# Kernel optimization log

Measured on AMD Instinct MI355X. Metric: run time of the kernel, lower is better.

The kernel has to match this reference:

```python
import jax, jax.numpy as jnp
import numpy as np

N = 100000   # nodes
E = 1000000  # edges
IN = 100     # input feature dim
H = 4        # heads
D = 32       # hidden per head (H*D = 128)
C = 47       # classes
EPS = 1e-5
SLOPE = 0.2  # DGL GATv2 leaky_relu negative slope


def setup_inputs() -> dict:
    key = jax.random.key(0)
    ks = jax.random.split(key, 32)
    lin = lambda k, i, o: (jax.random.normal(k, (i, o), jnp.float32) / np.float32(np.sqrt(i)))
    inp = {}
    inp['x'] = jax.random.normal(ks[0], (N, IN), jnp.float32)
    inp['src'] = jax.random.randint(ks[1], (E,), 0, N, jnp.int32)
    inp['dst'] = jnp.sort(jax.random.randint(ks[2], (E,), 0, N, jnp.int32))
    # layer 0: IN -> H*D, Linear residual (IN != H*D)
    inp['Wsrc0'] = lin(ks[3], IN, H * D); inp['bsrc0'] = jnp.zeros(H * D, jnp.float32)
    inp['Wdst0'] = lin(ks[4], IN, H * D); inp['bdst0'] = jnp.zeros(H * D, jnp.float32)
    inp['attn0'] = lin(ks[5], H, D)
    inp['Wres0'] = lin(ks[6], IN, H * D); inp['bres0'] = jnp.zeros(H * D, jnp.float32)
    # layer 1: H*D -> H*D, Identity residual (128 == 128)
    inp['Wsrc1'] = lin(ks[7], H * D, H * D); inp['bsrc1'] = jnp.zeros(H * D, jnp.float32)
    inp['Wdst1'] = lin(ks[8], H * D, H * D); inp['bdst1'] = jnp.zeros(H * D, jnp.float32)
    inp['attn1'] = lin(ks[9], H, D)
    # layer 2: H*D -> H*C, Linear residual (128 != 188)
    inp['Wsrc2'] = lin(ks[10], H * D, H * C); inp['bsrc2'] = jnp.zeros(H * C, jnp.float32)
    inp['Wdst2'] = lin(ks[11], H * D, H * C); inp['bdst2'] = jnp.zeros(H * C, jnp.float32)
    inp['attn2'] = lin(ks[12], H, C)
    inp['Wres2'] = lin(ks[13], H * D, H * C); inp['bres2'] = jnp.zeros(H * C, jnp.float32)
    # BatchNorm1d params (training-mode batch stats)
    inp['g0'] = jnp.ones(H * D, jnp.float32); inp['be0'] = jnp.zeros(H * D, jnp.float32)
    inp['g1'] = jnp.ones(H * D, jnp.float32); inp['be1'] = jnp.zeros(H * D, jnp.float32)
    return inp


def _gatv2(h, src, dst, Ws, bs, Wd, bd, attn, resval):
    """One GATv2Conv on a full block (src feats == dst feats == h)."""
    Hh, Dd = attn.shape
    fs = (h @ Ws + bs).reshape(-1, Hh, Dd)   # [N,H,D] src projection
    fd = (h @ Wd + bd).reshape(-1, Hh, Dd)   # [N,H,D] dst projection
    e = jax.nn.leaky_relu(fs[src] + fd[dst], SLOPE)         # [E,H,D]
    logits = jnp.einsum('ehd,hd->eh', e, attn)              # [E,H]
    m = jax.ops.segment_max(logits, dst, num_segments=N)    # per-dst max
    ex = jnp.exp(logits - m[dst])
    s = jax.ops.segment_sum(ex, dst, num_segments=N)
    alpha = ex / s[dst]                                      # edge softmax
    out = jax.ops.segment_sum(alpha[:, :, None] * fs[src], dst, num_segments=N)
    return out + resval                                      # [N,H,D]


def _bn(x, g, b):
    mu = x.mean(0)
    v = x.var(0)  # biased, as torch BN training mode
    return g * (x - mu) / jnp.sqrt(v + EPS) + b


def reference(x, src, dst,
              Wsrc0, bsrc0, Wdst0, bdst0, attn0, Wres0, bres0,
              Wsrc1, bsrc1, Wdst1, bdst1, attn1,
              Wsrc2, bsrc2, Wdst2, bdst2, attn2, Wres2, bres2,
              g0, be0, g1, be1):
    # layer 0: conv(+relu activation) -> flatten -> BN -> relu (dropout = eval identity)
    res0 = (x @ Wres0 + bres0).reshape(N, H, D)
    h = jax.nn.relu(_gatv2(x, src, dst, Wsrc0, bsrc0, Wdst0, bdst0, attn0, res0))
    h = jax.nn.relu(_bn(h.reshape(N, H * D), g0, be0))
    # layer 1: Identity residual
    res1 = h.reshape(N, H, D)
    h = jax.nn.relu(_gatv2(h, src, dst, Wsrc1, bsrc1, Wdst1, bdst1, attn1, res1))
    h = jax.nn.relu(_bn(h.reshape(N, H * D), g1, be1))
    # layer 2: no activation; mean over heads; log_softmax
    res2 = (h @ Wres2 + bres2).reshape(N, H, C)
    h = _gatv2(h, src, dst, Wsrc2, bsrc2, Wdst2, bdst2, attn2, res2)
    h = h.mean(1)                                # [N,C]
    return jax.nn.log_softmax(h, axis=-1)
```

## Files before the change

kernel.cpp:

```cpp
#include <hip/hip_runtime.h>
#include <hip/hip_bf16.h>

#define Nn 100000
#define Ee 1000000
#define INF_ 100
#define Hh 4
#define Dd 32
#define HD 128
#define Cc 47
#define HC 188
#define HCP 192
#define EPSV 1e-5f
#define SLOPE 0.2f
#define NBLK ((Nn + 255) / 256)

typedef __hip_bfloat16 bf16;
typedef __attribute__((ext_vector_type(8))) short short8;
typedef __attribute__((ext_vector_type(4))) float f32x4;
typedef __attribute__((ext_vector_type(2))) float f32x2;

__device__ __forceinline__ float tof(bf16 v) { return __bfloat162float(v); }
__device__ __forceinline__ float b2f(unsigned short u) {
    return __uint_as_float((unsigned)u << 16);
}
__device__ __forceinline__ float b2flo(unsigned u) {
    return __uint_as_float(u << 16);
}
__device__ __forceinline__ float b2fhi(unsigned u) {
    return __uint_as_float(u & 0xFFFF0000u);
}
__device__ __forceinline__ float ldb(const bf16* p) {
    return b2f(*(const unsigned short*)p);
}
__device__ __forceinline__ unsigned short f2u(float v) {
    bf16 t = __float2bfloat16(v);
    return *(unsigned short*)&t;
}
__device__ __forceinline__ f32x2 pk2(float x, float y) {
    f32x2 r; r.x = x; r.y = y; return r;
}
__device__ __forceinline__ f32x2 pabs2(f32x2 v) {
    return __builtin_elementwise_max(v, -v);
}
__device__ __forceinline__ f32x2 pfma2(f32x2 a, f32x2 b, f32x2 c) {
    return __builtin_elementwise_fma(a, b, c);
}

template <int C>
__device__ __forceinline__ float dppadd(float v) {
    int m = __builtin_amdgcn_update_dpp(0, __float_as_int(v), C, 0xF, 0xF, false);
    return v + __int_as_float(m);
}
template <int C>
__device__ __forceinline__ float dppmax(float v) {
    int m = __builtin_amdgcn_update_dpp(0, __float_as_int(v), C, 0xF, 0xF, false);
    return fmaxf(v, __int_as_float(m));
}
__device__ __forceinline__ float sum16(float p) {
    p = dppadd<0xB1>(p);
    p = dppadd<0x4E>(p);
    p = dppadd<0x124>(p);
    p = dppadd<0x128>(p);
    return p;
}
__device__ __forceinline__ float max16(float p) {
    p = dppmax<0xB1>(p); p = dppmax<0x4E>(p);
    p = dppmax<0x124>(p); p = dppmax<0x128>(p);
    return p;
}

#define L2E 1.4426950408889634f

__global__ void detect_dtype(const unsigned* __restrict__ x, int* __restrict__ flag) {
    if (blockIdx.x == 0 && threadIdx.x == 0) {
        int good = 0;
        for (int i = 0; i < 256; ++i) {
            unsigned lo = x[i] & 0xFFFFu;
            float v = __uint_as_float(lo << 16);
            float a = fabsf(v);
            if (a > 1e-4f && a < 10.f) good++;
        }
        *flag = (good >= 128) ? 1 : 0;
    }
}

__device__ __forceinline__ float ld_any(const void* p, int i, int isbf) {
    return isbf ? tof(((const bf16*)p)[i]) : ((const float*)p)[i];
}

__global__ void cvt_x(const void* __restrict__ in, bf16* __restrict__ out,
                      const int* __restrict__ flag) {
    int i = blockIdx.x * blockDim.x + threadIdx.x;
    if (i >= Nn * 128) return;
    int row = i >> 7, col = i & 127;
    float v = (col < INF_) ? ld_any(in, row * INF_ + col, *flag) : 0.f;
    out[i] = __float2bfloat16(v);
}

#define NSP 15
struct CvtTab { const void* src[NSP]; int off[NSP + 1]; };

__global__ void cvt_params(CvtTab t, bf16* __restrict__ out, int total,
                           const int* __restrict__ flag) {
    int i = blockIdx.x * blockDim.x + threadIdx.x;
    if (i >= total) return;
    int isbf = *flag;
    int seg = 0;
    while (i >= t.off[seg + 1]) seg++;
    out[i] = __float2bfloat16(ld_any(t.src[seg], i - t.off[seg], isbf));
}

#define WROWS 1280
struct PrepTab { const void* src[8]; int row0[8]; int K[8]; int M[8]; int MP[8]; };

__global__ void prep_all(PrepTab t, bf16* __restrict__ wtb, const int* __restrict__ flag) {
    int i = blockIdx.x * blockDim.x + threadIdx.x;
    if (i >= WROWS * 128) return;
    int row = i >> 7, k = i & 127;
    int isbf = *flag;
    float v = 0.f;
#pragma unroll
    for (int q = 0; q < 8; ++q) {
        if (row >= t.row0[q] && row < t.row0[q] + t.MP[q]) {
            int m = row - t.row0[q];
            if (m < t.M[q] && k < t.K[q])
                v = ld_any(t.src[q], k * t.M[q] + m, isbf);
        }
    }
    wtb[i] = __float2bfloat16(v);
}

__global__ void zero_u32(unsigned* __restrict__ p, int n) {
    int i = blockIdx.x * blockDim.x + threadIdx.x;
    if (i < n) p[i] = 0u;
}

__global__ void src_scale_ptr(const int* __restrict__ src, const int* __restrict__ dst,
                              unsigned* __restrict__ w384, unsigned* __restrict__ w256,
                              int* __restrict__ ptr) {
    int i = blockIdx.x * blockDim.x + threadIdx.x;
    if (i < Ee) {
        unsigned s = (unsigned)src[i];
        w384[i] = s * 384u;
        w256[i] = s << 8;
    }
    if (i <= Nn) {
        if (i == Nn) { ptr[Nn] = Ee; return; }
        int lo = 0, hi = Ee;
        while (lo < hi) {
            int mid = (lo + hi) >> 1;
            if (dst[mid] < i) lo = mid + 1; else hi = mid;
        }
        ptr[i] = lo;
    }
}

__global__ void deg_hist_blk(const int* __restrict__ ptr, int* __restrict__ cnt) {
    __shared__ int lh[256];
    int t = threadIdx.x;
    lh[t] = 0;
    __syncthreads();
    int n = blockIdx.x * 256 + t;
    if (n < Nn) {
        int dg = ptr[n + 1] - ptr[n]; if (dg > 255) dg = 255;
        atomicAdd(&lh[dg], 1);
    }
    __syncthreads();
    cnt[t * NBLK + blockIdx.x] = lh[t];
}

__global__ void deg_totals(const int* __restrict__ cnt, int* __restrict__ totals) {
    int wave = threadIdx.x >> 6, lane = threadIdx.x & 63;
    int bin = blockIdx.x * 4 + wave;
    int s = 0;
    for (int k = lane; k < NBLK; k += 64) s += cnt[bin * NBLK + k];
#pragma unroll
    for (int o = 1; o < 64; o <<= 1) s += __shfl_xor(s, o);
    if (lane == 0) totals[bin] = s;
}

__global__ void deg_bases(const int* __restrict__ cnt, const int* __restrict__ totals,
                          int* __restrict__ base) {
    int wave = threadIdx.x >> 6, lane = threadIdx.x & 63;
    int bin = blockIdx.x * 4 + wave;
    int bb = 0;
    for (int b = bin + 1 + lane; b < 256; b += 64) bb += totals[b];
#pragma unroll
    for (int o = 1; o < 64; o <<= 1) bb += __shfl_xor(bb, o);
    int run = bb;
    for (int k0 = 0; k0 < NBLK; k0 += 64) {
        int k = k0 + lane;
        int c = (k < NBLK) ? cnt[bin * NBLK + k] : 0;
        int p = c;
#pragma unroll
        for (int o = 1; o < 64; o <<= 1) {
            int t = __shfl_up(p, o);
            if (lane >= o) p += t;
        }
        if (k < NBLK) base[bin * NBLK + k] = run + (p - c);
        run += __shfl(p, 63);
    }
}

__global__ void deg_scatter_blk(const int* __restrict__ ptr, const int* __restrict__ base,
                                int* __restrict__ perm) {
    __shared__ int lh[256];
    int t = threadIdx.x;
    lh[t] = 0;
    __syncthreads();
    int n = blockIdx.x * 256 + t;
    if (n < Nn) {
        int dg = ptr[n + 1] - ptr[n]; if (dg > 255) dg = 255;
        int loc = atomicAdd(&lh[dg], 1);
        perm[base[dg * NBLK + blockIdx.x] + loc] = n;
    }
}

template <int MP, int NOUT, int CS, bool ABN, bool PACK, int OSTR>
__global__ __launch_bounds__(256, 4) void gemm_big(
    const bf16* __restrict__ A, const bf16* __restrict__ Wt,
    const bf16* __restrict__ b0, const bf16* __restrict__ b1,
    const bf16* __restrict__ b2,
    bf16* __restrict__ o0, bf16* __restrict__ o1, bf16* __restrict__ o2,
    int MR, const float* __restrict__ bnp) {
    __shared__ __align__(16) bf16 Al[64 * 136];
    const int row0 = blockIdx.x * 64;
    const int tid = threadIdx.x;
#pragma unroll
    for (int j = 0; j < 4; ++j) {
        int idx = tid + j * 256;
        int r = idx >> 4, kk = (idx & 15) * 8;
        int4 val = {0, 0, 0, 0};
        if (row0 + r < Nn) {
            val = *(const int4*)&A[(size_t)(row0 + r) * 128 + kk];
            if (ABN) {
                short8 av = *(short8*)&val;
                bf16 tmp[8];
#pragma unroll
                for (int u = 0; u < 8; ++u) {
                    float v = b2f((unsigned short)av[u]);
                    v = fmaxf(fmaf(v, bnp[kk + u], bnp[128 + kk + u]), 0.f);
                    tmp[u] = __float2bfloat16(v);
                }
                val = *(int4*)tmp;
            }
        }
        *(int4*)&Al[r * 136 + kk] = val;
    }
    __syncthreads();
    const int wave = tid >> 6, lane = tid & 63;
    const int n16 = lane & 15, quad = lane >> 4;
    const int colbase = blockIdx.y * (64 * CS) + wave * (16 * CS);
    f32x4 acc[4][CS];
#pragma unroll
    for (int rt = 0; rt < 4; ++rt)
#pragma unroll
        for (int c = 0; c < CS; ++c) acc[rt][c] = (f32x4){0.f, 0.f, 0.f, 0.f};
    const bf16* wb[CS];
#pragma unroll
    for (int c = 0; c < CS; ++c)
        wb[c] = Wt + (size_t)(colbase + c * 16 + n16) * 128 + quad * 8;
    const bf16* ap = Al + n16 * 136 + quad * 8;
#pragma unroll
    for (int ks = 0; ks < 4; ++ks) {
        short8 bf[CS];
#pragma unroll
        for (int c = 0; c < CS; ++c) bf[c] = *(const short8*)(wb[c] + ks * 32);
#pragma unroll
        for (int rt = 0; rt < 4; ++rt) {
            short8 af = *(const short8*)(ap + rt * 16 * 136 + ks * 32);
#pragma unroll
            for (int c = 0; c < CS; ++c)
                acc[rt][c] = __builtin_amdgcn_mfma_f32_16x16x32_bf16(af, bf[c], acc[rt][c], 0, 0, 0);
        }
    }
#pragma unroll
    for (int c = 0; c < CS; ++c) {
        int col = colbase + c * 16 + n16;
        int oi = col / MP, lc = col - oi * MP;
        if (oi >= NOUT || lc >= MR) continue;
        const bf16* bp = (oi == 0) ? b0 : (oi == 1) ? b1 : b2;
        bf16* o = (oi == 0) ? o0 : (oi == 1) ? o1 : o2;
        float bb = tof(bp[lc]);
        int st;
        if (PACK) {
            int hh = lc / 47, cc = lc - hh * 47;
            int jj = cc & 15, kk2 = cc >> 4;
            int l = hh * 16 + jj;
            st = (kk2 < 2) ? (2 * l + kk2) : (128 + l);
        } else {
            st = lc;
        }
#pragma unroll
        for (int rt = 0; rt < 4; ++rt) {
#pragma unroll
            for (int i = 0; i < 4; ++i) {
                int row = row0 + rt * 16 + quad * 4 + i;
                if (row < Nn)
                    o[(size_t)row * OSTR + st] = __float2bfloat16(acc[rt][c][i] + bb);
            }
        }
    }
}

template <bool RESBN>
__global__ __launch_bounds__(256) void gat_fused_128(
    const bf16* __restrict__ fs, const bf16* __restrict__ fd,
    const unsigned* __restrict__ srcW, const int* __restrict__ ptr,
    const int* __restrict__ perm,
    const bf16* __restrict__ attn, const bf16* __restrict__ resb,
    const float* __restrict__ bnp, bf16* __restrict__ hout) {
    const int wave = threadIdx.x >> 6, lane = threadIdx.x & 63;
    const int di = blockIdx.x * 4 + wave;
    if (di >= Nn) return;
    const int d = perm[di];
    const int c0 = lane * 2;
    const unsigned c0b = (unsigned)c0 * 2u;
    ushort2 aq = *(const ushort2*)&attn[c0];
    float a0 = b2f(aq.x) * L2E, a1 = b2f(aq.y) * L2E;
    const f32x2 Av = pk2(0.6f * a0, 0.6f * a1);
    const f32x2 Bv = pk2(0.4f * a0, 0.4f * a1);
    ushort2 dq = *(const ushort2*)&fd[(size_t)d * HD + c0];
    const f32x2 fdv = pk2(b2f(dq.x), b2f(dq.y));
    const char* fsb = (const char*)fs;
    float l = 0.f;
    f32x2 Ov = pk2(0.f, 0.f);
    int e = ptr[d];
    const int e1 = ptr[d + 1];
    for (; e + 3 < e1; e += 4) {
        unsigned vA = srcW[e] + c0b, vB = srcW[e + 1] + c0b;
        unsigned vC = srcW[e + 2] + c0b, vD = srcW[e + 3] + c0b;
        ushort2 qA = *(const ushort2*)(fsb + vA);
        ushort2 qB = *(const ushort2*)(fsb + vB);
        ushort2 qC = *(const ushort2*)(fsb + vC);
        ushort2 qD = *(const ushort2*)(fsb + vD);
        f32x2 fA = pk2(b2f(qA.x), b2f(qA.y));
        f32x2 fB = pk2(b2f(qB.x), b2f(qB.y));
        f32x2 fC = pk2(b2f(qC.x), b2f(qC.y));
        f32x2 fD = pk2(b2f(qD.x), b2f(qD.y));
        f32x2 xA = fA + fdv, xB = fB + fdv, xC = fC + fdv, xD = fD + fdv;
        f32x2 tA = pfma2(pabs2(xA), Bv, xA * Av);
        f32x2 tB = pfma2(pabs2(xB), Bv, xB * Av);
        f32x2 tC = pfma2(pabs2(xC), Bv, xC * Av);
        f32x2 tD = pfma2(pabs2(xD), Bv, xD * Av);
        float pA = tA.x + tA.y, pB = tB.x + tB.y;
        float pC = tC.x + tC.y, pD = tD.x + tD.y;
        pA = sum16(pA); pB = sum16(pB); pC = sum16(pC); pD = sum16(pD);
        float eA = __builtin_amdgcn_exp2f(pA), eB = __builtin_amdgcn_exp2f(pB);
        float eC = __builtin_amdgcn_exp2f(pC), eD = __builtin_amdgcn_exp2f(pD);
        l += (eA + eB) + (eC + eD);
        Ov = pfma2(pk2(eA, eA), fA, Ov);
        Ov = pfma2(pk2(eB, eB), fB, Ov);
        Ov = pfma2(pk2(eC, eC), fC, Ov);
        Ov = pfma2(pk2(eD, eD), fD, Ov);
    }
    for (; e < e1; ++e) {
        unsigned v = srcW[e] + c0b;
        ushort2 fq = *(const ushort2*)(fsb + v);
        f32x2 f = pk2(b2f(fq.x), b2f(fq.y));
        f32x2 x = f + fdv;
        f32x2 t = pfma2(pabs2(x), Bv, x * Av);
        float p = sum16(t.x + t.y);
        float pe = __builtin_amdgcn_exp2f(p);
        l += pe;
        Ov = pfma2(pk2(pe, pe), f, Ov);
    }
    float inv = l > 0.f ? 1.f / l : 0.f;
    ushort2 rq = *(const ushort2*)&resb[(size_t)d * HD + c0];
    float r0 = b2f(rq.x), r1 = b2f(rq.y);
    if (RESBN) {
        r0 = fmaxf(fmaf(r0, bnp[c0], bnp[HD + c0]), 0.f);
        r1 = fmaxf(fmaf(r1, bnp[c0 + 1], bnp[HD + c0 + 1]), 0.f);
    }
    float v0 = fmaxf(fmaf(Ov.x, inv, r0), 0.f);
    float v1 = fmaxf(fmaf(Ov.y, inv, r1), 0.f);
    ushort2 ov; ov.x = f2u(v0); ov.y = f2u(v1);
    *(ushort2*)&hout[(size_t)d * HD + c0] = ov;
}

__global__ __launch_bounds__(256) void gat_fused_188(
    const bf16* __restrict__ fs, const bf16* __restrict__ fd,
    const unsigned* __restrict__ srcW, const int* __restrict__ ptr,
    const int* __restrict__ perm,
    const bf16* __restrict__ attn, const bf16* __restrict__ rs,
    void* __restrict__ out, const int* __restrict__ flag) {
    const int wave = threadIdx.x >> 6, lane = threadIdx.x & 63;
    const int di = blockIdx.x * 4 + wave;
    if (di >= Nn) return;
    const int d = perm[di];
    const int h = lane >> 4, j = lane & 15;
    const unsigned cbA = (unsigned)lane * 4u;
    const unsigned cbB = 256u + (unsigned)lane * 2u;
    const int ca = h * Cc + j;
    const bool has2 = (j < 15);
    float a0 = ldb(&attn[ca]) * L2E;
    float a1 = ldb(&attn[ca + 16]) * L2E;
    float a2 = has2 ? ldb(&attn[ca + 32]) * L2E : 0.f;
    const f32x2 Av = pk2(0.6f * a0, 0.6f * a1);
    const f32x2 Bv = pk2(0.4f * a0, 0.4f * a1);
    const float A2 = 0.6f * a2, B2 = 0.4f * a2;
    const char* fdb = (const char*)fd;
    const size_t drow = (size_t)d * 384u;
    unsigned dqa = *(const unsigned*)(fdb + drow + cbA);
    unsigned short dqb = *(const unsigned short*)(fdb + drow + cbB);
    const f32x2 fdv = pk2(b2flo(dqa), b2fhi(dqa));
    const float fd2 = b2f(dqb);
    const char* fsb = (const char*)fs;
    float l = 0.f, O2 = 0.f;
    f32x2 Ov = pk2(0.f, 0.f);
    int e = ptr[d];
    const int e1 = ptr[d + 1];
    for (; e + 3 < e1; e += 4) {
        unsigned bA = srcW[e], bB = srcW[e + 1], bC = srcW[e + 2], bD = srcW[e + 3];
        unsigned qA = *(const unsigned*)(fsb + bA + cbA);
        unsigned qB = *(const unsigned*)(fsb + bB + cbA);
        unsigned qC = *(const unsigned*)(fsb + bC + cbA);
        unsigned qD = *(const unsigned*)(fsb + bD + cbA);
        unsigned short uA = *(const unsigned short*)(fsb + bA + cbB);
        unsigned short uB = *(const unsigned short*)(fsb + bB + cbB);
        unsigned short uC = *(const unsigned short*)(fsb + bC + cbB);
        unsigned short uD = *(const unsigned short*)(fsb + bD + cbB);
        f32x2 fA = pk2(b2flo(qA), b2fhi(qA)); float gA = b2f(uA);
        f32x2 fB = pk2(b2flo(qB), b2fhi(qB)); float gB = b2f(uB);
        f32x2 fC = pk2(b2flo(qC), b2fhi(qC)); float gC = b2f(uC);
        f32x2 fD = pk2(b2flo(qD), b2fhi(qD)); float gD = b2f(uD);
        f32x2 xA = fA + fdv, xB = fB + fdv, xC = fC + fdv, xD = fD + fdv;
        float yA = gA + fd2, yB = gB + fd2, yC = gC + fd2, yD = gD + fd2;
        f32x2 tA = pfma2(pabs2(xA), Bv, xA * Av);
        f32x2 tB = pfma2(pabs2(xB), Bv, xB * Av);
        f32x2 tC = pfma2(pabs2(xC), Bv, xC * Av);
        f32x2 tD = pfma2(pabs2(xD), Bv, xD * Av);
        float pA = fmaf(yA, A2, fmaf(fabsf(yA), B2, tA.x + tA.y));
        float pB = fmaf(yB, A2, fmaf(fabsf(yB), B2, tB.x + tB.y));
        float pC = fmaf(yC, A2, fmaf(fabsf(yC), B2, tC.x + tC.y));
        float pD = fmaf(yD, A2, fmaf(fabsf(yD), B2, tD.x + tD.y));
        pA = sum16(pA); pB = sum16(pB); pC = sum16(pC); pD = sum16(pD);
        float eA = __builtin_amdgcn_exp2f(pA), eB = __builtin_amdgcn_exp2f(pB);
        float eC = __builtin_amdgcn_exp2f(pC), eD = __builtin_amdgcn_exp2f(pD);
        l += (eA + eB) + (eC + eD);
        Ov = pfma2(pk2(eA, eA), fA, Ov); O2 = fmaf(eA, gA, O2);
        Ov = pfma2(pk2(eB, eB), fB, Ov); O2 = fmaf(eB, gB, O2);
        Ov = pfma2(pk2(eC, eC), fC, Ov); O2 = fmaf(eC, gC, O2);
        Ov = pfma2(pk2(eD, eD), fD, Ov); O2 = fmaf(eD, gD, O2);
    }
    for (; e < e1; ++e) {
        unsigned b = srcW[e];
        unsigned q = *(const unsigned*)(fsb + b + cbA);
        unsigned short u = *(const unsigned short*)(fsb + b + cbB);
        f32x2 f = pk2(b2flo(q), b2fhi(q)); float g = b2f(u);
        f32x2 x = f + fdv;
        float y = g + fd2;
        f32x2 t = pfma2(pabs2(x), Bv, x * Av);
        float p = fmaf(y, A2, fmaf(fabsf(y), B2, t.x + t.y));
        p = sum16(p);
        float pe = __builtin_amdgcn_exp2f(p);
        l += pe;
        Ov = pfma2(pk2(pe, pe), f, Ov); O2 = fmaf(pe, g, O2);
    }
    float inv = l > 0.f ? 1.f / l : 0.f;
    const char* rb_ = (const char*)rs;
    unsigned rqa = *(const unsigned*)(rb_ + drow + cbA);
    unsigned short rqb = *(const unsigned short*)(rb_ + drow + cbB);
    float v0 = fmaf(Ov.x, inv, b2flo(rqa));
    float v1 = fmaf(Ov.y, inv, b2fhi(rqa));
    float v2 = has2 ? fmaf(O2, inv, b2f(rqb)) : 0.f;
    v0 += __shfl_xor(v0, 16); v0 += __shfl_xor(v0, 32); v0 *= 0.25f;
    v1 += __shfl_xor(v1, 16); v1 += __shfl_xor(v1, 32); v1 *= 0.25f;
    v2 += __shfl_xor(v2, 16); v2 += __shfl_xor(v2, 32); v2 *= 0.25f;
    float mx = fmaxf(v0, v1);
    if (has2) mx = fmaxf(mx, v2);
    mx = max16(mx);
    float sm = __expf(v0 - mx) + __expf(v1 - mx) + (has2 ? __expf(v2 - mx) : 0.f);
    sm = sum16(sm);
    if (h == 0) {
        float ls = mx + logf(sm);
        if (*flag) {
            bf16* o = (bf16*)out + (size_t)d * Cc;
            o[j] = __float2bfloat16(v0 - ls);
            o[j + 16] = __float2bfloat16(v1 - ls);
            if (has2) o[j + 32] = __float2bfloat16(v2 - ls);
        } else {
            float* o = (float*)out + (size_t)d * Cc;
            o[j] = v0 - ls;
            o[j + 16] = v1 - ls;
            if (has2) o[j + 32] = v2 - ls;
        }
    }
}

__global__ void col_stats(const bf16* __restrict__ in, float* __restrict__ sums) {
    int c = threadIdx.x;
    int r0 = blockIdx.x * 256;
    int r1 = r0 + 256; if (r1 > Nn) r1 = Nn;
    float s = 0.f, s2 = 0.f;
    for (int r = r0; r < r1; ++r) {
        float v = ldb(&in[(size_t)r * HD + c]);
        s += v; s2 += v * v;
    }
    atomicAdd(&sums[c], s);
    atomicAdd(&sums[HD + c], s2);
}

__global__ void bn_finalize(const float* __restrict__ sums, const bf16* __restrict__ g,
                            const bf16* __restrict__ be, float* __restrict__ ss) {
    int c = threadIdx.x;
    float mu = sums[c] * (1.f / Nn);
    float var = sums[HD + c] * (1.f / Nn) - mu * mu;
    float sc = tof(g[c]) * rsqrtf(var + EPSV);
    ss[c] = sc;
    ss[HD + c] = tof(be[c]) - mu * sc;
}

extern "C" void kernel_launch(void* const* d_in, const int* in_sizes, int n_in,
                              void* d_out, int out_size, void* d_ws, size_t ws_size,
                              hipStream_t stream) {
    (void)in_sizes; (void)n_in; (void)out_size; (void)ws_size;
    const void* x = d_in[0];
    const int* src = (const int*)d_in[1];
    const int* dst = (const int*)d_in[2];

    char* ws = (char*)d_ws;
    size_t off = 0;
    auto alloc = [&](size_t bytes) {
        void* p = ws + off;
        off += (bytes + 255) & ~(size_t)255;
        return p;
    };
    bf16* xb = (bf16*)alloc((size_t)Nn * 128 * 2);
    bf16* rb = (bf16*)alloc((size_t)Nn * HD * 2);
    bf16* rs = xb;
    bf16* fs = (bf16*)alloc((size_t)Nn * HCP * 2);
    bf16* fd = (bf16*)alloc((size_t)Nn * HCP * 2);
    bf16* hbA = (bf16*)alloc((size_t)Nn * HD * 2);
    bf16* hbB = (bf16*)alloc((size_t)Nn * HD * 2);
    int* ptr = (int*)alloc((Nn + 1) * 4);
    bf16* wtb = (bf16*)alloc((size_t)WROWS * 128 * 2);
    float* bns = (float*)alloc(2 * HD * 4);
    float* bnss0 = (float*)alloc(2 * HD * 4);
    float* bnss1 = (float*)alloc(2 * HD * 4);
    bf16* pb = (bf16*)alloc(4096 * 2);
    int* flag = (int*)alloc(256);
    unsigned* w384 = (unsigned*)alloc((size_t)Ee * 4);
    unsigned* w256 = (unsigned*)alloc((size_t)Ee * 4);
    int* cnt = (int*)alloc((size_t)256 * NBLK * 4);
    int* cbase = (int*)alloc((size_t)256 * NBLK * 4);
    int* totals = (int*)alloc(256 * 4);
    int* perm = (int*)alloc((size_t)Nn * 4);

    static const int spIdx[NSP] = {4, 6, 7, 9, 11, 13, 14, 16, 18, 19, 21, 22, 23, 24, 25};
    static const int spSz[NSP]  = {HD, HD, HD, HD, HD, HD, HD, HC, HC, HC, HC, HD, HD, HD, HD};
    CvtTab tab;
    int tot = 0;
    for (int i = 0; i < NSP; ++i) { tab.src[i] = d_in[spIdx[i]]; tab.off[i] = tot; tot += spSz[i]; }
    tab.off[NSP] = tot;
    const bf16 *bsrc0 = pb + tab.off[0], *bdst0 = pb + tab.off[1], *attn0 = pb + tab.off[2],
               *bres0 = pb + tab.off[3], *bsrc1 = pb + tab.off[4], *bdst1 = pb + tab.off[5],
               *attn1 = pb + tab.off[6], *bsrc2 = pb + tab.off[7], *bdst2 = pb + tab.off[8],
               *attn2 = pb + tab.off[9], *bres2 = pb + tab.off[10],
               *g0 = pb + tab.off[11], *be0 = pb + tab.off[12],
               *g1 = pb + tab.off[13], *be1 = pb + tab.off[14];

    PrepTab pt;
    static const int wIdx[8] = {3, 5, 8, 10, 12, 15, 17, 20};
    static const int wK[8]   = {INF_, INF_, INF_, HD, HD, HD, HD, HD};
    static const int wM[8]   = {HD, HD, HD, HD, HD, HC, HC, HC};
    static const int wMP[8]  = {128, 128, 128, 128, 128, 192, 192, 192};
    static const int wR0[8]  = {0, 128, 256, 384, 512, 640, 832, 1024};
    for (int i = 0; i < 8; ++i) {
        pt.src[i] = d_in[wIdx[i]]; pt.row0[i] = wR0[i];
        pt.K[i] = wK[i]; pt.M[i] = wM[i]; pt.MP[i] = wMP[i];
    }

    detect_dtype<<<1, 64, 0, stream>>>((const unsigned*)x, flag);
    cvt_x<<<(Nn * 128 + 255) / 256, 256, 0, stream>>>(x, xb, flag);
    cvt_params<<<(tot + 255) / 256, 256, 0, stream>>>(tab, pb, tot, flag);
    prep_all<<<(WROWS * 128 + 255) / 256, 256, 0, stream>>>(pt, wtb, flag);
    src_scale_ptr<<<(Ee + 255) / 256, 256, 0, stream>>>(src, dst, w384, w256, ptr);
    deg_hist_blk<<<NBLK, 256, 0, stream>>>(ptr, cnt);
    deg_totals<<<64, 256, 0, stream>>>(cnt, totals);
    deg_bases<<<64, 256, 0, stream>>>(cnt, totals, cbase);
    deg_scatter_blk<<<NBLK, 256, 0, stream>>>(ptr, cbase, perm);

    const int fusedGrid = (Nn + 3) / 4;
    const int statsGrid = NBLK;
    const int rowBlk = (Nn + 63) / 64;

    gemm_big<128, 3, 3, false, false, HD><<<dim3(rowBlk, 2), 256, 0, stream>>>(
        xb, wtb, bsrc0, bdst0, bres0, fs, fd, rb, HD, nullptr);
    gat_fused_128<false><<<fusedGrid, 256, 0, stream>>>(fs, fd, w256, ptr, perm,
                                                        attn0, rb, nullptr, hbA);
    zero_u32<<<1, 256, 0, stream>>>((unsigned*)bns, 2 * HD);
    col_stats<<<statsGrid, 128, 0, stream>>>(hbA, bns);
    bn_finalize<<<1, HD, 0, stream>>>(bns, g0, be0, bnss0);

    gemm_big<128, 2, 2, true, false, HD><<<dim3(rowBlk, 2), 256, 0, stream>>>(
        hbA, wtb + (size_t)384 * 128, bsrc1, bdst1, nullptr, fs, fd, nullptr, HD, bnss0);
    gat_fused_128<true><<<fusedGrid, 256, 0, stream>>>(fs, fd, w256, ptr, perm,
                                                       attn1, hbA, bnss0, hbB);
    zero_u32<<<1, 256, 0, stream>>>((unsigned*)bns, 2 * HD);
    col_stats<<<statsGrid, 128, 0, stream>>>(hbB, bns);
    bn_finalize<<<1, HD, 0, stream>>>(bns, g1, be1, bnss1);

    gemm_big<192, 3, 3, true, true, HCP><<<dim3(rowBlk, 3), 256, 0, stream>>>(
        hbB, wtb + (size_t)640 * 128, bsrc2, bdst2, bres2, fs, fd, rs, HC, bnss1);
    gat_fused_188<<<fusedGrid, 256, 0, stream>>>(fs, fd, w384, ptr, perm, attn2, rs,
                                                 d_out, flag);
}
```

Before: 663.9 us.

## Loop column tiles inside GEMM blocks, vectorize edge index loads, use fast log

The GEMM kernel now loops over all column tiles inside one block rather than spreading them across grid.y. The A tile is loaded, and BN-transformed, into LDS once per row block instead of once per column tile, at the cost of a smaller grid and more serial work per block. The GAT aggregation kernels peel edges until the index is 4-aligned so the four source indices can be read with one uint4 load. The final log_softmax uses __log2f times ln2 in place of logf.

```diff
diff --git a/kernel.cpp b/kernel.cpp
--- a/kernel.cpp
+++ b/kernel.cpp
@@ -70,6 +70,7 @@
 }
 
 #define L2E 1.4426950408889634f
+#define LN2 0.6931471805599453f
 
 __global__ void detect_dtype(const unsigned* __restrict__ x, int* __restrict__ flag) {
     if (blockIdx.x == 0 && threadIdx.x == 0) {
@@ -216,7 +217,7 @@
     }
 }
 
-template <int MP, int NOUT, int CS, bool ABN, bool PACK, int OSTR>
+template <int MP, int NOUT, int CS, bool ABN, bool PACK, int OSTR, int NY>
 __global__ __launch_bounds__(256, 4) void gemm_big(
     const bf16* __restrict__ A, const bf16* __restrict__ Wt,
     const bf16* __restrict__ b0, const bf16* __restrict__ b1,
@@ -250,54 +251,57 @@
     __syncthreads();
     const int wave = tid >> 6, lane = tid & 63;
     const int n16 = lane & 15, quad = lane >> 4;
-    const int colbase = blockIdx.y * (64 * CS) + wave * (16 * CS);
-    f32x4 acc[4][CS];
-#pragma unroll
-    for (int rt = 0; rt < 4; ++rt)
-#pragma unroll
-        for (int c = 0; c < CS; ++c) acc[rt][c] = (f32x4){0.f, 0.f, 0.f, 0.f};
-    const bf16* wb[CS];
-#pragma unroll
-    for (int c = 0; c < CS; ++c)
-        wb[c] = Wt + (size_t)(colbase + c * 16 + n16) * 128 + quad * 8;
     const bf16* ap = Al + n16 * 136 + quad * 8;
 #pragma unroll
-    for (int ks = 0; ks < 4; ++ks) {
-        short8 bf[CS];
-#pragma unroll
-        for (int c = 0; c < CS; ++c) bf[c] = *(const short8*)(wb[c] + ks * 32);
-#pragma unroll
-        for (int rt = 0; rt < 4; ++rt) {
-            short8 af = *(const short8*)(ap + rt * 16 * 136 + ks * 32);
-#pragma unroll
-            for (int c = 0; c < CS; ++c)
-                acc[rt][c] = __builtin_amdgcn_mfma_f32_16x16x32_bf16(af, bf[c], acc[rt][c], 0, 0, 0);
-        }
-    }
-#pragma unroll
-    for (int c = 0; c < CS; ++c) {
-        int col = colbase + c * 16 + n16;
-        int oi = col / MP, lc = col - oi * MP;
-        if (oi >= NOUT || lc >= MR) continue;
-        const bf16* bp = (oi == 0) ? b0 : (oi == 1) ? b1 : b2;
-        bf16* o = (oi == 0) ? o0 : (oi == 1) ? o1 : o2;
-        float bb = tof(bp[lc]);
-        int st;
-        if (PACK) {
-            int hh = lc / 47, cc = lc - hh * 47;
-            int jj = cc & 15, kk2 = cc >> 4;
-            int l = hh * 16 + jj;
-            st = (kk2 < 2) ? (2 * l + kk2) : (128 + l);
-        } else {
-            st = lc;
-        }
-#pragma unroll
-        for (int rt = 0; rt < 4; ++rt) {
-#pragma unroll
-            for (int i = 0; i < 4; ++i) {
-                int row = row0 + rt * 16 + quad * 4 + i;
-                if (row < Nn)
-                    o[(size_t)row * OSTR + st] = __float2bfloat16(acc[rt][c][i] + bb);
+    for (int ny = 0; ny < NY; ++ny) {
+        const int colbase = ny * (64 * CS) + wave * (16 * CS);
+        f32x4 acc[4][CS];
+#pragma unroll
+        for (int rt = 0; rt < 4; ++rt)
+#pragma unroll
+            for (int c = 0; c < CS; ++c) acc[rt][c] = (f32x4){0.f, 0.f, 0.f, 0.f};
+        const bf16* wb[CS];
+#pragma unroll
+        for (int c = 0; c < CS; ++c)
+            wb[c] = Wt + (size_t)(colbase + c * 16 + n16) * 128 + quad * 8;
+#pragma unroll
+        for (int ks = 0; ks < 4; ++ks) {
+            short8 bf[CS];
+#pragma unroll
+            for (int c = 0; c < CS; ++c) bf[c] = *(const short8*)(wb[c] + ks * 32);
+#pragma unroll
+            for (int rt = 0; rt < 4; ++rt) {
+                short8 af = *(const short8*)(ap + rt * 16 * 136 + ks * 32);
+#pragma unroll
+                for (int c = 0; c < CS; ++c)
+                    acc[rt][c] = __builtin_amdgcn_mfma_f32_16x16x32_bf16(af, bf[c], acc[rt][c], 0, 0, 0);
+            }
+        }
+#pragma unroll
+        for (int c = 0; c < CS; ++c) {
+            int col = colbase + c * 16 + n16;
+            int oi = col / MP, lc = col - oi * MP;
+            if (oi >= NOUT || lc >= MR) continue;
+            const bf16* bp = (oi == 0) ? b0 : (oi == 1) ? b1 : b2;
+            bf16* o = (oi == 0) ? o0 : (oi == 1) ? o1 : o2;
+            float bb = tof(bp[lc]);
+            int st;
+            if (PACK) {
+                int hh = lc / 47, cc = lc - hh * 47;
+                int jj = cc & 15, kk2 = cc >> 4;
+                int l = hh * 16 + jj;
+                st = (kk2 < 2) ? (2 * l + kk2) : (128 + l);
+            } else {
+                st = lc;
+            }
+#pragma unroll
+            for (int rt = 0; rt < 4; ++rt) {
+#pragma unroll
+                for (int i = 0; i < 4; ++i) {
+                    int row = row0 + rt * 16 + quad * 4 + i;
+                    if (row < Nn)
+                        o[(size_t)row * OSTR + st] = __float2bfloat16(acc[rt][c][i] + bb);
+                }
             }
         }
     }
@@ -327,9 +331,21 @@
     f32x2 Ov = pk2(0.f, 0.f);
     int e = ptr[d];
     const int e1 = ptr[d + 1];
+    for (; e < e1 && (e & 3); ++e) {
+        unsigned v = srcW[e] + c0b;
+        ushort2 fq = *(const ushort2*)(fsb + v);
+        f32x2 f = pk2(b2f(fq.x), b2f(fq.y));
+        f32x2 x = f + fdv;
+        f32x2 t = pfma2(pabs2(x), Bv, x * Av);
+        float p = sum16(t.x + t.y);
+        float pe = __builtin_amdgcn_exp2f(p);
+        l += pe;
+        Ov = pfma2(pk2(pe, pe), f, Ov);
+    }
     for (; e + 3 < e1; e += 4) {
-        unsigned vA = srcW[e] + c0b, vB = srcW[e + 1] + c0b;
-        unsigned vC = srcW[e + 2] + c0b, vD = srcW[e + 3] + c0b;
+        uint4 sw = *(const uint4*)&srcW[e];
+        unsigned vA = sw.x + c0b, vB = sw.y + c0b;
+        unsigned vC = sw.z + c0b, vD = sw.w + c0b;
         ushort2 qA = *(const ushort2*)(fsb + vA);
         ushort2 qB = *(const ushort2*)(fsb + vB);
         ushort2 qC = *(const ushort2*)(fsb + vC);
@@ -410,8 +426,23 @@
     f32x2 Ov = pk2(0.f, 0.f);
     int e = ptr[d];
     const int e1 = ptr[d + 1];
+    for (; e < e1 && (e & 3); ++e) {
+        unsigned b = srcW[e];
+        unsigned q = *(const unsigned*)(fsb + b + cbA);
+        unsigned short u = *(const unsigned short*)(fsb + b + cbB);
+        f32x2 f = pk2(b2flo(q), b2fhi(q)); float g = b2f(u);
+        f32x2 x = f + fdv;
+        float y = g + fd2;
+        f32x2 t = pfma2(pabs2(x), Bv, x * Av);
+        float p = fmaf(y, A2, fmaf(fabsf(y), B2, t.x + t.y));
+        p = sum16(p);
+        float pe = __builtin_amdgcn_exp2f(p);
+        l += pe;
+        Ov = pfma2(pk2(pe, pe), f, Ov); O2 = fmaf(pe, g, O2);
+    }
     for (; e + 3 < e1; e += 4) {
-        unsigned bA = srcW[e], bB = srcW[e + 1], bC = srcW[e + 2], bD = srcW[e + 3];
+        uint4 sw = *(const uint4*)&srcW[e];
+        unsigned bA = sw.x, bB = sw.y, bC = sw.z, bD = sw.w;
         unsigned qA = *(const unsigned*)(fsb + bA + cbA);
         unsigned qB = *(const unsigned*)(fsb + bB + cbA);
         unsigned qC = *(const unsigned*)(fsb + bC + cbA);
@@ -473,7 +504,7 @@
     float sm = __expf(v0 - mx) + __expf(v1 - mx) + (has2 ? __expf(v2 - mx) : 0.f);
     sm = sum16(sm);
     if (h == 0) {
-        float ls = mx + logf(sm);
+        float ls = mx + __log2f(sm) * LN2;
         if (*flag) {
             bf16* o = (bf16*)out + (size_t)d * Cc;
             o[j] = __float2bfloat16(v0 - ls);
@@ -585,7 +616,7 @@
     const int statsGrid = NBLK;
     const int rowBlk = (Nn + 63) / 64;
 
-    gemm_big<128, 3, 3, false, false, HD><<<dim3(rowBlk, 2), 256, 0, stream>>>(
+    gemm_big<128, 3, 3, false, false, HD, 2><<<rowBlk, 256, 0, stream>>>(
         xb, wtb, bsrc0, bdst0, bres0, fs, fd, rb, HD, nullptr);
     gat_fused_128<false><<<fusedGrid, 256, 0, stream>>>(fs, fd, w256, ptr, perm,
                                                         attn0, rb, nullptr, hbA);
@@ -593,7 +624,7 @@
     col_stats<<<statsGrid, 128, 0, stream>>>(hbA, bns);
     bn_finalize<<<1, HD, 0, stream>>>(bns, g0, be0, bnss0);
 
-    gemm_big<128, 2, 2, true, false, HD><<<dim3(rowBlk, 2), 256, 0, stream>>>(
+    gemm_big<128, 2, 2, true, false, HD, 2><<<rowBlk, 256, 0, stream>>>(
         hbA, wtb + (size_t)384 * 128, bsrc1, bdst1, nullptr, fs, fd, nullptr, HD, bnss0);
     gat_fused_128<true><<<fusedGrid, 256, 0, stream>>>(fs, fd, w256, ptr, perm,
                                                        attn1, hbA, bnss0, hbB);
@@ -601,7 +632,7 @@
     col_stats<<<statsGrid, 128, 0, stream>>>(hbB, bns);
     bn_finalize<<<1, HD, 0, stream>>>(bns, g1, be1, bnss1);
 
-    gemm_big<192, 3, 3, true, true, HCP><<<dim3(rowBlk, 3), 256, 0, stream>>>(
+    gemm_big<192, 3, 3, true, true, HCP, 3><<<rowBlk, 256, 0, stream>>>(
         hbB, wtb + (size_t)640 * 128, bsrc2, bdst2, bres2, fs, fd, rs, HC, bnss1);
     gat_fused_188<<<fusedGrid, 256, 0, stream>>>(fs, fd, w384, ptr, perm, attn2, rs,
                                                  d_out, flag);
```

After: 704.8 us. 1.06x slower.
